# Optimization experiments

Hardware: AMD Instinct MI355X
Metric: run time of the kernel (lower is better)

The kernel has to match this reference:

```python
import jax, jax.numpy as jnp
import numpy as np

D_MODEL = 2048
D_STATE = 16
D_CONV = 4
EXPAND = 2
D_INNER = EXPAND * D_MODEL  # 4096
BATCH = 32768


def setup_inputs() -> dict:
    key = jax.random.key(0)
    ks = jax.random.split(key, 8)
    x = jax.random.normal(ks[0], (BATCH, D_MODEL), dtype=jnp.float32)
    in_w = jax.random.normal(ks[1], (D_MODEL, D_INNER), dtype=jnp.float32) * 0.02
    in_b = jnp.zeros((D_INNER,), jnp.float32)
    # depthwise conv kernel: (d_inner, d_conv) (groups == channels, so in-chan dim is 1)
    conv_w = jax.random.normal(ks[2], (D_INNER, D_CONV), dtype=jnp.float32) * 0.1
    conv_b = jnp.zeros((D_INNER,), jnp.float32)
    # A = log(arange(1, d_state+1)) broadcast to (d_inner, d_state), as in __init__
    A_log = jnp.log(jnp.broadcast_to(
        jnp.arange(1, D_STATE + 1, dtype=jnp.float32), (D_INNER, D_STATE)))
    B = jax.random.normal(ks[3], (D_INNER, D_STATE), dtype=jnp.float32)
    C = jax.random.normal(ks[4], (D_INNER, D_STATE), dtype=jnp.float32)
    Dp = jnp.ones((D_INNER,), jnp.float32)
    dt = jnp.ones((D_INNER,), jnp.float32)
    out_w = jax.random.normal(ks[5], (D_INNER, D_MODEL), dtype=jnp.float32) * 0.02
    out_b = jnp.zeros((D_MODEL,), jnp.float32)
    return dict(x=x, in_w=in_w, in_b=in_b, conv_w=conv_w, conv_b=conv_b,
                A_log=A_log, B=B, C=C, Dp=Dp, dt=dt, out_w=out_w, out_b=out_b)


def reference(x, in_w, in_b, conv_w, conv_b, A_log, B, C, Dp, dt, out_w, out_b):
    # in_proj: (batch, d_model) -> (batch, d_inner)
    xi = x @ in_w + in_b

    # Depthwise causal Conv1d(kernel=d_conv, padding=d_conv-1) on a length-1
    # sequence; torch takes x_conv[:, :, :1]. Output position 0 sees (d_conv-1)
    # left-pad zeros followed by x, so only the LAST kernel tap contributes:
    x_conv = xi * conv_w[:, -1] + conv_b  # (batch, d_inner)

    # Single-step selective scan with zero initial state:
    #   delta = softplus(dt);  A = -exp(A_log)
    #   h = exp(delta*A) * h0 + delta * B * u  (h0 = 0 => exp term vanishes)
    #   y = sum_n C[:,n] * h[:,:,n] + D * u
    # which reduces per-channel to: y = u * (delta * sum_n(B*C) + D)
    delta = jax.nn.softplus(dt)                       # (d_inner,)
    A = -jnp.exp(A_log)                               # (d_inner, d_state) (cancels with h0=0)
    del A
    bc = jnp.sum(B * C, axis=-1)                      # (d_inner,)
    y = xi * (delta * bc + Dp)                        # (batch, d_inner)

    out = jax.nn.silu(x_conv + y)                     # SiLU gate
    return out @ out_w + out_b                        # (batch, d_model)
```

## Files before the change

### kernel.cpp

```cpp
#include <hip/hip_runtime.h>
#include <stdint.h>
#include <stddef.h>

#define D_MODEL 2048
#define D_INNER 4096

typedef float f32x4 __attribute__((ext_vector_type(4)));
typedef short short8 __attribute__((ext_vector_type(8)));
typedef __bf16 bf16x8 __attribute__((ext_vector_type(8)));

static __device__ __forceinline__ unsigned short f32_to_bf16(float f){
  unsigned int u = __builtin_bit_cast(unsigned int, f);
  u += 0x7FFFu + ((u >> 16) & 1u);
  return (unsigned short)(u >> 16);
}

static __device__ __forceinline__ f32x4 mfma_bf16(short8 a, short8 b, f32x4 c){
  return __builtin_amdgcn_mfma_f32_16x16x32_bf16(
      __builtin_bit_cast(bf16x8, a), __builtin_bit_cast(bf16x8, b), c, 0, 0, 0);
}

static __device__ __forceinline__ void gload_lds16(const void* g, void* l){
  __builtin_amdgcn_global_load_lds(
      (const __attribute__((address_space(1))) void*)g,
      (__attribute__((address_space(3))) void*)l, 16, 0, 0);
}

#define BARF() do { asm volatile("" ::: "memory"); \
                    __builtin_amdgcn_s_barrier();  \
                    asm volatile("" ::: "memory"); } while(0)

__global__ void prep_coef_k(const float* __restrict__ conv_w, const float* __restrict__ Bm,
                            const float* __restrict__ Cm, const float* __restrict__ Dp,
                            const float* __restrict__ dt, float* __restrict__ coef){
  int c = blockIdx.x * 256 + threadIdx.x;
  if (c >= D_INNER) return;
  float d = dt[c];
  float sp = (d > 20.f) ? d : log1pf(__expf(d));
  float bc = 0.f;
  #pragma unroll
  for (int n = 0; n < 16; n++) bc += Bm[c*16+n] * Cm[c*16+n];
  coef[c] = conv_w[c*4+3] + sp * bc + Dp[c];
}

__global__ void transpose_cvt_k(const float* __restrict__ in, unsigned short* __restrict__ outT,
                                int K, int N){
  __shared__ float t[32][33];
  int n0 = blockIdx.x * 32, k0 = blockIdx.y * 32;
  int tx = threadIdx.x, ty = threadIdx.y;
  #pragma unroll
  for (int i = 0; i < 4; i++)
    t[ty + 8*i][tx] = in[(size_t)(k0 + ty + 8*i) * N + n0 + tx];
  __syncthreads();
  #pragma unroll
  for (int i = 0; i < 4; i++)
    outT[(size_t)(n0 + ty + 8*i) * K + k0 + tx] = f32_to_bf16(t[tx][ty + 8*i]);
}

__global__ void cvt_x_k(const float4* __restrict__ x, ushort4* __restrict__ xb, int n4){
  int stride = gridDim.x * blockDim.x;
  for (int i = blockIdx.x * blockDim.x + threadIdx.x; i < n4; i += stride){
    float4 v = x[i];
    ushort4 o;
    o.x = f32_to_bf16(v.x); o.y = f32_to_bf16(v.y);
    o.z = f32_to_bf16(v.z); o.w = f32_to_bf16(v.w);
    xb[i] = o;
  }
}

template<int EPI>
__global__ __launch_bounds__(512, 2) void gemm8_k(
    const unsigned short* __restrict__ A,
    const unsigned short* __restrict__ Bt,
    int M, int N, int K,
    const float* __restrict__ bias,
    const float* __restrict__ coef,
    const float* __restrict__ convb,
    unsigned short* __restrict__ gate,
    float* __restrict__ out)
{
  __shared__ __align__(16) unsigned short smem[65536];
  char* ldsc = (char*)smem;

  const int tid = threadIdx.x;
  const int wid = tid >> 6, lane = tid & 63;
  const int wr = wid >> 2, wc = wid & 3;
  const int l15 = lane & 15, lg = lane >> 4;

  const int nbx = N >> 8;
  const int cpx = gridDim.x >> 3;
  const int bid = blockIdx.x;
  const int swz = (bid & 7) * cpx + (bid >> 3);
  const int mb = swz / nbx, nb = swz % nbx;
  const int m0 = mb << 8, n0 = nb << 8;

  const int cswz = lg ^ ((l15 >> 1) & 3);
  const int aoff = (wr*128 + l15)*64 + cswz*16;
  const int boff = (wc*64  + l15)*64 + cswz*16;

  const int s0 = wid*128 + lane;
  const int s1 = s0 + 64;
  const int r0 = s0 >> 2, r1 = s1 >> 2;
  const int c0 = (s0 & 3) ^ ((r0 >> 1) & 3);
  const int c1 = (s1 & 3) ^ ((r1 >> 1) & 3);
  const unsigned short* pA0 = A  + (size_t)(m0 + r0)*K + c0*8;
  const unsigned short* pA1 = A  + (size_t)(m0 + r1)*K + c1*8;
  const unsigned short* pB0 = Bt + (size_t)(n0 + r0)*K + c0*8;
  const unsigned short* pB1 = Bt + (size_t)(n0 + r1)*K + c1*8;

  const int ntile = K >> 6;

#define STAGE_(ST, SKS, SMAT) do {                                          \
    int st_ = (ST); if (st_ > ntile-1) st_ = ntile-1;                       \
    const int ktks_ = st_*64 + (SKS)*32;                                    \
    unsigned short* reg_ = smem + ((st_ & 1) << 15) + ((SMAT) << 14) + ((SKS) << 13); \
    if ((SMAT) == 0) {                                                      \
      gload_lds16(pA0 + ktks_, reg_ + s0*8);                                \
      gload_lds16(pA1 + ktks_, reg_ + s1*8);                                \
    } else {                                                                \
      gload_lds16(pB0 + ktks_, reg_ + s0*8);                                \
      gload_lds16(pB1 + ktks_, reg_ + s1*8);                                \
    }                                                                       \
  } while(0)

  f32x4 acc[8][4];
  #pragma unroll
  for (int i = 0; i < 8; i++)
    #pragma unroll
    for (int j = 0; j < 4; j++)
      #pragma unroll
      for (int r = 0; r < 4; r++) acc[i][j][r] = 0.f;
  short8 af[8];

  STAGE_(0,0,0); STAGE_(0,0,1); STAGE_(0,1,0); STAGE_(0,1,1);
  STAGE_(1,0,0); STAGE_(1,0,1);
  asm volatile("s_waitcnt vmcnt(4)" ::: "memory");
  __builtin_amdgcn_s_barrier();

#define CPH_(H, KS, STT, SKS, DOVM) do {                                    \
    const char* regA_ = ldsc + (H)*65536 + (KS)*16384;                      \
    const char* regB_ = regA_ + 32768;                                      \
    _Pragma("unroll")                                                       \
    for (int mi_ = 0; mi_ < 8; ++mi_)                                       \
      af[mi_] = *(const short8*)(regA_ + aoff + mi_*1024);                  \
    const short8 bb0_ = *(const short8*)(regB_ + boff);                     \
    const short8 bb1_ = *(const short8*)(regB_ + boff + 1024);              \
    const short8 bb2_ = *(const short8*)(regB_ + boff + 2048);              \
    const short8 bb3_ = *(const short8*)(regB_ + boff + 3072);              \
    STAGE_(t + (STT), SKS, 0);                                              \
    STAGE_(t + (STT), SKS, 1);                                              \
    __builtin_amdgcn_s_setprio(1);                                          \
    _Pragma("unroll")                                                       \
    for (int mi_ = 0; mi_ < 8; ++mi_) {                                     \
      acc[mi_][0] = mfma_bf16(af[mi_], bb0_, acc[mi_][0]);                  \
      acc[mi_][1] = mfma_bf16(af[mi_], bb1_, acc[mi_][1]);                  \
      acc[mi_][2] = mfma_bf16(af[mi_], bb2_, acc[mi_][2]);                  \
      acc[mi_][3] = mfma_bf16(af[mi_], bb3_, acc[mi_][3]);                  \
    }                                                                       \
    __builtin_amdgcn_s_setprio(0);                                          \
    if (DOVM) { asm volatile("s_waitcnt vmcnt(4)" ::: "memory"); }          \
    BARF();                                                                 \
  } while(0)

  const int niter = ntile >> 1;
  #pragma unroll 1
  for (int it = 0; it < niter; ++it) {
    const int t = it << 1;
    CPH_(0, 0, 1, 1, 0);
    CPH_(0, 1, 2, 0, 1);
    CPH_(1, 0, 2, 1, 0);
    CPH_(1, 1, 3, 0, 1);
  }
#undef CPH_
#undef STAGE_

  asm volatile("s_waitcnt vmcnt(0)" ::: "memory");
  BARF();

  const int lrow = lg << 2;
  if (EPI == 0){
    unsigned short* st = smem;
    #pragma unroll
    for (int p = 0; p < 2; ++p){
      if (wr == p){
        #pragma unroll
        for (int ni = 0; ni < 4; ++ni){
          const int col = wc*64 + ni*16 + l15;
          const int gcol = n0 + col;
          const float ib = bias[gcol], cf = coef[gcol], cb = convb[gcol];
          #pragma unroll
          for (int mi = 0; mi < 8; ++mi){
            const int rl = mi*16 + lrow;
            #pragma unroll
            for (int r = 0; r < 4; ++r){
              float z = (acc[mi][ni][r] + ib) * cf + cb;
              float g = z / (1.f + __expf(-z));
              st[(rl + r)*264 + col] = f32_to_bf16(g);
            }
          }
        }
      }
      BARF();
      #pragma unroll
      for (int rd = 0; rd < 8; ++rd){
        const int idx = rd*512 + tid;
        const int row = idx >> 5, c8 = (idx & 31) << 3;
        short8 v = *(const short8*)&st[row*264 + c8];
        *(short8*)&gate[(size_t)(m0 + p*128 + row) * N + n0 + c8] = v;
      }
      BARF();
    }
  } else {
    float* stf = (float*)smem;
    #pragma unroll
    for (int p = 0; p < 4; ++p){
      if (wr == (p >> 1)){
        #pragma unroll
        for (int ni = 0; ni < 4; ++ni){
          const int col = wc*64 + ni*16 + l15;
          const float ob = bias[n0 + col];
          #pragma unroll
          for (int mi2 = 0; mi2 < 4; ++mi2){
            const int mi = (p & 1)*4 + mi2;
            const int rl = mi2*16 + lrow;
            #pragma unroll
            for (int r = 0; r < 4; ++r)
              stf[(rl + r)*260 + col] = acc[mi][ni][r] + ob;
          }
        }
      }
      BARF();
      #pragma unroll
      for (int rd = 0; rd < 8; ++rd){
        const int idx = rd*512 + tid;
        const int row = idx >> 6, c4 = (idx & 63) << 2;
        f32x4 v = *(const f32x4*)&stf[row*260 + c4];
        *(f32x4*)&out[(size_t)(m0 + p*64 + row) * N + n0 + c4] = v;
      }
      BARF();
    }
  }
}

#define BM 128
#define BN 128
#define BK 64

__global__ __launch_bounds__(256) void gemm_bt_f32a_k(
    const float* __restrict__ A32, const unsigned short* __restrict__ Bt,
    int M, int N, int K,
    const float* __restrict__ bias,
    const float* __restrict__ coef,
    const float* __restrict__ convb,
    unsigned short* __restrict__ gate)
{
  __shared__ __align__(16) unsigned short lsA[BM*BK];
  __shared__ __align__(16) unsigned short lsB[BN*BK];
  const int tid = threadIdx.x;
  const int wid = tid >> 6, lane = tid & 63;
  const int wr = wid >> 1, wc = wid & 1;
  const int nbx = N / BN;
  const int cpx = gridDim.x >> 3;
  const int bid = blockIdx.x;
  const int swz = (bid & 7) * cpx + (bid >> 3);
  const int m0 = (swz / nbx) * BM, n0 = (swz % nbx) * BN;

  f32x4 acc[4][4];
  #pragma unroll
  for (int i = 0; i < 4; i++)
    #pragma unroll
    for (int j = 0; j < 4; j++)
      #pragma unroll
      for (int r = 0; r < 4; r++) acc[i][j][r] = 0.f;

  for (int kt = 0; kt < K; kt += BK){
    __syncthreads();
    #pragma unroll
    for (int i = 0; i < 8; i++){
      int c = tid + i*256;
      int row = c >> 4, c4 = (c & 15) << 2;
      const float4 v = *(const float4*)&A32[(size_t)(m0+row)*K + kt + c4];
      ushort4 o;
      o.x = f32_to_bf16(v.x); o.y = f32_to_bf16(v.y);
      o.z = f32_to_bf16(v.z); o.w = f32_to_bf16(v.w);
      *(ushort4*)&lsA[row*BK + c4] = o;
    }
    #pragma unroll
    for (int i = 0; i < 4; i++){
      int c = (wid*4 + i)*64 + lane;
      int row = c >> 3, c8 = (c & 7) << 3;
      gload_lds16(&Bt[(size_t)(n0+row)*K + kt + c8], &lsB[c*8]);
    }
    __syncthreads();

    #pragma unroll
    for (int ks = 0; ks < 2; ks++){
      short8 af[4], bf[4];
      const int ko = ks*32 + ((lane >> 4) << 3);
      #pragma unroll
      for (int mi = 0; mi < 4; mi++)
        af[mi] = *(const short8*)&lsA[(wr*64 + mi*16 + (lane & 15))*BK + ko];
      #pragma unroll
      for (int ni = 0; ni < 4; ni++)
        bf[ni] = *(const short8*)&lsB[(wc*64 + ni*16 + (lane & 15))*BK + ko];
      #pragma unroll
      for (int mi = 0; mi < 4; mi++)
        #pragma unroll
        for (int ni = 0; ni < 4; ni++)
          acc[mi][ni] = mfma_bf16(af[mi], bf[ni], acc[mi][ni]);
    }
  }

  const int lrow = (lane >> 4) << 2;
  const int lcol = lane & 15;
  #pragma unroll
  for (int ni = 0; ni < 4; ni++){
    int col = n0 + wc*64 + ni*16 + lcol;
    float ib = bias[col], cf = coef[col], cb = convb[col];
    #pragma unroll
    for (int mi = 0; mi < 4; mi++){
      int rb = m0 + wr*64 + mi*16 + lrow;
      #pragma unroll
      for (int r = 0; r < 4; r++){
        float z = (acc[mi][ni][r] + ib) * cf + cb;
        float g = z / (1.f + __expf(-z));
        gate[(size_t)(rb + r) * N + col] = f32_to_bf16(g);
      }
    }
  }
}

extern "C" void kernel_launch(void* const* d_in, const int* in_sizes, int n_in,
                              void* d_out, int out_size, void* d_ws, size_t ws_size,
                              hipStream_t stream){
  const float* x      = (const float*)d_in[0];
  const float* in_w   = (const float*)d_in[1];
  const float* in_b   = (const float*)d_in[2];
  const float* conv_w = (const float*)d_in[3];
  const float* conv_b = (const float*)d_in[4];
  const float* Bm     = (const float*)d_in[6];
  const float* Cm     = (const float*)d_in[7];
  const float* Dp     = (const float*)d_in[8];
  const float* dt     = (const float*)d_in[9];
  const float* out_w  = (const float*)d_in[10];
  const float* out_b  = (const float*)d_in[11];

  const int M = in_sizes[0] / D_MODEL;

  char* ws = (char*)d_ws;
  const size_t gate_sz = (size_t)M * D_INNER * 2;
  const size_t w1t_off = gate_sz;
  const size_t w1t_sz  = (size_t)D_MODEL * D_INNER * 2;
  const size_t w2t_off = w1t_off + w1t_sz;
  const size_t w2t_sz  = (size_t)D_INNER * D_MODEL * 2;
  const size_t coef_off = w2t_off + w2t_sz;
  const size_t coef_sz  = (size_t)D_INNER * 4;
  const size_t xb_off   = (coef_off + coef_sz + 255) & ~(size_t)255;
  const size_t xb_sz    = (size_t)M * D_MODEL * 2;

  unsigned short* gate = (unsigned short*)ws;
  unsigned short* w1t  = (unsigned short*)(ws + w1t_off);
  unsigned short* w2t  = (unsigned short*)(ws + w2t_off);
  float*          coef = (float*)(ws + coef_off);
  unsigned short* xb   = (unsigned short*)(ws + xb_off);
  const bool have_xb = ws_size >= xb_off + xb_sz;

  prep_coef_k<<<D_INNER/256, 256, 0, stream>>>(conv_w, Bm, Cm, Dp, dt, coef);
  transpose_cvt_k<<<dim3(D_INNER/32, D_MODEL/32), dim3(32,8), 0, stream>>>(in_w, w1t, D_MODEL, D_INNER);
  transpose_cvt_k<<<dim3(D_MODEL/32, D_INNER/32), dim3(32,8), 0, stream>>>(out_w, w2t, D_INNER, D_MODEL);
  if (have_xb)
    cvt_x_k<<<2048, 256, 0, stream>>>((const float4*)x, (ushort4*)xb, (M*D_MODEL)/4);

  if (have_xb){
    const int g1 = (M/256) * (D_INNER/256);
    gemm8_k<0><<<g1, 512, 0, stream>>>(xb, w1t, M, D_INNER, D_MODEL,
                                       in_b, coef, conv_b, gate, nullptr);
  } else {
    const int g1 = (M/BM) * (D_INNER/BN);
    gemm_bt_f32a_k<<<g1, 256, 0, stream>>>(x, w1t, M, D_INNER, D_MODEL,
                                           in_b, coef, conv_b, gate);
  }

  const int g2 = (M/256) * (D_MODEL/256);
  gemm8_k<1><<<g2, 512, 0, stream>>>(gate, w2t, M, D_MODEL, D_INNER,
                                     out_b, nullptr, nullptr, nullptr, (float*)d_out);
}
```

Before: 1.174 ms.

## Double-buffer LDS fragment registers to overlap next-phase reads with MFMAs

Splits the A/B fragment registers into two sets so each phase loads the next k-slice from LDS while issuing MFMAs on the previously loaded set, with a prologue load and a sched_barrier to keep ordering. Waits on vmcnt every phase instead of every other phase. Also switches epilogue global stores to nontemporal stores to avoid polluting cache. Costs extra VGPRs (another 12 short8 registers), which may cut occupancy or cause spills, and the more frequent vmcnt waits may stall.

```diff
diff --git a/kernel.cpp b/kernel.cpp
--- a/kernel.cpp
+++ b/kernel.cpp
@@ -130,35 +130,48 @@
     for (int j = 0; j < 4; j++)
       #pragma unroll
       for (int r = 0; r < 4; r++) acc[i][j][r] = 0.f;
-  short8 af[8];
+
+  short8 afX[8], afY[8], bbX[4], bbY[4];
 
   STAGE_(0,0,0); STAGE_(0,0,1); STAGE_(0,1,0); STAGE_(0,1,1);
   STAGE_(1,0,0); STAGE_(1,0,1);
   asm volatile("s_waitcnt vmcnt(4)" ::: "memory");
   __builtin_amdgcn_s_barrier();
-
-#define CPH_(H, KS, STT, SKS, DOVM) do {                                    \
-    const char* regA_ = ldsc + (H)*65536 + (KS)*16384;                      \
+  {
+    const char* regA_ = ldsc;
+    const char* regB_ = regA_ + 32768;
+    #pragma unroll
+    for (int mi_ = 0; mi_ < 8; ++mi_)
+      afX[mi_] = *(const short8*)(regA_ + aoff + mi_*1024);
+    bbX[0] = *(const short8*)(regB_ + boff);
+    bbX[1] = *(const short8*)(regB_ + boff + 1024);
+    bbX[2] = *(const short8*)(regB_ + boff + 2048);
+    bbX[3] = *(const short8*)(regB_ + boff + 3072);
+  }
+
+#define CPH_(CA, CB, NA, NB, RT, RKS, STT, SKS) do {                        \
+    const char* regA_ = ldsc + (((RT) & 1) << 16) + ((RKS) << 14);          \
     const char* regB_ = regA_ + 32768;                                      \
     _Pragma("unroll")                                                       \
     for (int mi_ = 0; mi_ < 8; ++mi_)                                       \
-      af[mi_] = *(const short8*)(regA_ + aoff + mi_*1024);                  \
-    const short8 bb0_ = *(const short8*)(regB_ + boff);                     \
-    const short8 bb1_ = *(const short8*)(regB_ + boff + 1024);              \
-    const short8 bb2_ = *(const short8*)(regB_ + boff + 2048);              \
-    const short8 bb3_ = *(const short8*)(regB_ + boff + 3072);              \
+      NA[mi_] = *(const short8*)(regA_ + aoff + mi_*1024);                  \
+    NB[0] = *(const short8*)(regB_ + boff);                                 \
+    NB[1] = *(const short8*)(regB_ + boff + 1024);                          \
+    NB[2] = *(const short8*)(regB_ + boff + 2048);                          \
+    NB[3] = *(const short8*)(regB_ + boff + 3072);                          \
     STAGE_(t + (STT), SKS, 0);                                              \
     STAGE_(t + (STT), SKS, 1);                                              \
+    __builtin_amdgcn_sched_barrier(0);                                      \
     __builtin_amdgcn_s_setprio(1);                                          \
     _Pragma("unroll")                                                       \
     for (int mi_ = 0; mi_ < 8; ++mi_) {                                     \
-      acc[mi_][0] = mfma_bf16(af[mi_], bb0_, acc[mi_][0]);                  \
-      acc[mi_][1] = mfma_bf16(af[mi_], bb1_, acc[mi_][1]);                  \
-      acc[mi_][2] = mfma_bf16(af[mi_], bb2_, acc[mi_][2]);                  \
-      acc[mi_][3] = mfma_bf16(af[mi_], bb3_, acc[mi_][3]);                  \
+      acc[mi_][0] = mfma_bf16(CA[mi_], CB[0], acc[mi_][0]);                 \
+      acc[mi_][1] = mfma_bf16(CA[mi_], CB[1], acc[mi_][1]);                 \
+      acc[mi_][2] = mfma_bf16(CA[mi_], CB[2], acc[mi_][2]);                 \
+      acc[mi_][3] = mfma_bf16(CA[mi_], CB[3], acc[mi_][3]);                 \
     }                                                                       \
     __builtin_amdgcn_s_setprio(0);                                          \
-    if (DOVM) { asm volatile("s_waitcnt vmcnt(4)" ::: "memory"); }          \
+    asm volatile("s_waitcnt vmcnt(4)" ::: "memory");                        \
     BARF();                                                                 \
   } while(0)
 
@@ -166,15 +179,16 @@
   #pragma unroll 1
   for (int it = 0; it < niter; ++it) {
     const int t = it << 1;
-    CPH_(0, 0, 1, 1, 0);
-    CPH_(0, 1, 2, 0, 1);
-    CPH_(1, 0, 2, 1, 0);
-    CPH_(1, 1, 3, 0, 1);
+    CPH_(afX, bbX, afY, bbY, t,   1, 1, 1);
+    CPH_(afY, bbY, afX, bbX, t+1, 0, 2, 0);
+    CPH_(afX, bbX, afY, bbY, t+1, 1, 2, 1);
+    CPH_(afY, bbY, afX, bbX, t+2, 0, 3, 0);
   }
 #undef CPH_
 #undef STAGE_
 
   asm volatile("s_waitcnt vmcnt(0)" ::: "memory");
+  asm volatile("s_waitcnt lgkmcnt(0)" ::: "memory");
   BARF();
 
   const int lrow = lg << 2;
@@ -206,7 +220,8 @@
         const int idx = rd*512 + tid;
         const int row = idx >> 5, c8 = (idx & 31) << 3;
         short8 v = *(const short8*)&st[row*264 + c8];
-        *(short8*)&gate[(size_t)(m0 + p*128 + row) * N + n0 + c8] = v;
+        __builtin_nontemporal_store(
+            v, (short8*)&gate[(size_t)(m0 + p*128 + row) * N + n0 + c8]);
       }
       BARF();
     }
@@ -235,7 +250,8 @@
         const int idx = rd*512 + tid;
         const int row = idx >> 6, c4 = (idx & 63) << 2;
         f32x4 v = *(const f32x4*)&stf[row*260 + c4];
-        *(f32x4*)&out[(size_t)(m0 + p*64 + row) * N + n0 + c4] = v;
+        __builtin_nontemporal_store(
+            v, (f32x4*)&out[(size_t)(m0 + p*64 + row) * N + n0 + c4]);
       }
       BARF();
     }
```

After: 1.140 ms. -2.9%, faster.
